# Kernel optimization log

Hardware: AMD Instinct MI355X
Metric: run time of the kernel (lower is better)

## Reference

```python
import jax, jax.numpy as jnp
import numpy as np

N_NODES = 30000
IN_DIM = 8
HIDDEN = 64
HEADS1 = 8
OUT_DIM = 8
NEG_SLOPE = 0.2


def _glorot(key, shape):
    fan_in, fan_out = shape[0], shape[-1]
    lim = jnp.sqrt(6.0 / (fan_in + fan_out))
    return jax.random.uniform(key, shape, jnp.float32, -lim, lim)


def setup_inputs() -> dict:
    key = jax.random.key(0)
    ks = jax.random.split(key, 12)
    x = jax.random.normal(ks[0], (N_NODES, IN_DIM), jnp.float32)
    edge_index = jax.random.randint(ks[1], (2, 300000), 0, N_NODES, jnp.int32)
    # layer 1: in=8, out=HIDDEN per head, 8 heads, concat
    W1l = _glorot(ks[2], (IN_DIM, HEADS1 * HIDDEN))
    W1r = _glorot(ks[3], (IN_DIM, HEADS1 * HIDDEN))
    a1 = _glorot(ks[4], (HEADS1, HIDDEN))
    b1 = jnp.zeros((HEADS1 * HIDDEN,), jnp.float32)
    # layer 2: in=HEADS1*HIDDEN, out=OUT_DIM, 1 head
    W2l = _glorot(ks[5], (HEADS1 * HIDDEN, OUT_DIM))
    W2r = _glorot(ks[6], (HEADS1 * HIDDEN, OUT_DIM))
    a2 = _glorot(ks[7], (1, OUT_DIM))
    b2 = jnp.zeros((OUT_DIM,), jnp.float32)
    return {"x": x, "edge_index": edge_index, "W1l": W1l, "W1r": W1r,
            "a1": a1, "b1": b1, "W2l": W2l, "W2r": W2r, "a2": a2, "b2": b2}


def gatv2_layer(x, src, dst, Wl, Wr, att, bias, heads, out_ch):
    n = x.shape[0]
    xl = (x @ Wl).reshape(n, heads, out_ch)   # messages (source side)
    xr = (x @ Wr).reshape(n, heads, out_ch)   # target side
    h = jax.nn.leaky_relu(xl[src] + xr[dst], NEG_SLOPE)   # [E,H,C]
    e = jnp.einsum('ehc,hc->eh', h, att)                  # [E,H]
    # segment softmax over incoming edges per destination node
    m = jax.ops.segment_max(e, dst, num_segments=n)
    p = jnp.exp(e - m[dst])
    denom = jax.ops.segment_sum(p, dst, num_segments=n)
    alpha = p / denom[dst]                                # [E,H]
    out = jax.ops.segment_sum(alpha[..., None] * xl[src], dst, num_segments=n)
    return out.reshape(n, heads * out_ch) + bias


def reference(x, edge_index, W1l, W1r, a1, b1, W2l, W2r, a2, b2):
    n = x.shape[0]
    loops = jnp.arange(n, dtype=edge_index.dtype)
    src = jnp.concatenate([edge_index[0], loops])  # add_self_loops=True (PyG default)
    dst = jnp.concatenate([edge_index[1], loops])
    h = gatv2_layer(x, src, dst, W1l, W1r, a1, b1, HEADS1, HIDDEN)
    h = jax.nn.relu(h)
    out = gatv2_layer(h, src, dst, W2l, W2r, a2, b2, 1, OUT_DIM)
    return out
```

## Files before the change

kernel.cpp:

```cpp
#include <hip/hip_runtime.h>
#include <math.h>

#define N_NODES   30000
#define N_EDGE    300000
#define N_EDGE_T  330000
#define HEADS     8
#define HIDDEN    64
#define IN_DIM    8
#define OUT_DIM   8
#define NEG_SLOPE 0.2f

typedef float v2f __attribute__((ext_vector_type(2)));


__global__ __launch_bounds__(256) void count_kernel(const int* __restrict__ ei,
                                                    int* __restrict__ count) {
    int e = blockIdx.x * 256 + threadIdx.x;
    if (e >= N_EDGE_T) return;
    int d = (e < N_EDGE) ? ei[N_EDGE + e] : (e - N_EDGE);
    atomicAdd(&count[d], 1);
}

__global__ __launch_bounds__(1024) void scan_kernel(const int* __restrict__ count,
                                                    int* __restrict__ row_start,
                                                    int* __restrict__ cursor) {
    __shared__ int wsum[16];
    const int tid  = threadIdx.x;
    const int wave = tid >> 6;
    const int lane = tid & 63;
    const int4* c4 = (const int4*)count;
    const int N4 = N_NODES / 4;
    int run = 0;
    for (int r = 0; r < 4; ++r) {
        const int g  = r * 1024 + tid;
        const int i0 = 2 * g;
        const int i1 = 2 * g + 1;
        int4 v0 = make_int4(0,0,0,0), v1 = make_int4(0,0,0,0);
        if (i0 < N4) v0 = c4[i0];
        if (i1 < N4) v1 = c4[i1];
        int s = v0.x + v0.y + v0.z + v0.w + v1.x + v1.y + v1.z + v1.w;
        int sc = s;
        #pragma unroll
        for (int off = 1; off < 64; off <<= 1) {
            int t = __shfl_up(sc, off, 64);
            if (lane >= off) sc += t;
        }
        if (lane == 63) wsum[wave] = sc;
        __syncthreads();
        if (tid < 16) {
            int w = wsum[tid];
            #pragma unroll
            for (int off = 1; off < 16; off <<= 1) {
                int t = __shfl_up(w, off, 64);
                if (tid >= off) w += t;
            }
            wsum[tid] = w;
        }
        __syncthreads();
        const int woff = (wave > 0) ? wsum[wave - 1] : 0;
        int e0 = run + woff + (sc - s);
        int4 ex0, ex1;
        ex0.x = e0;           ex0.y = ex0.x + v0.x;
        ex0.z = ex0.y + v0.y; ex0.w = ex0.z + v0.z;
        int e4 = ex0.w + v0.w;
        ex1.x = e4;           ex1.y = ex1.x + v1.x;
        ex1.z = ex1.y + v1.y; ex1.w = ex1.z + v1.z;
        if (i0 < N4) { ((int4*)row_start)[i0] = ex0; ((int4*)cursor)[i0] = ex0; }
        if (i1 < N4) { ((int4*)row_start)[i1] = ex1; ((int4*)cursor)[i1] = ex1; }
        const int tot = wsum[15];
        __syncthreads();
        run += tot;
    }
    if (tid == 0) row_start[N_NODES] = run;
}

__global__ __launch_bounds__(256) void scatter_kernel(const int* __restrict__ ei,
                                                      int* __restrict__ cursor,
                                                      int* __restrict__ edge_src,
                                                      const float* __restrict__ x,
                                                      float* __restrict__ xg) {
    int e = blockIdx.x * 256 + threadIdx.x;
    if (e >= N_EDGE_T) return;
    int s, d;
    if (e < N_EDGE) { s = ei[e]; d = ei[N_EDGE + e]; }
    else            { s = d = e - N_EDGE; }
    int pos = atomicAdd(&cursor[d], 1);
    edge_src[pos] = s;
    const float4* xs = (const float4*)(x + s * IN_DIM);
    float4 a = xs[0], b = xs[1];
    float4* dst = (float4*)(xg + pos * IN_DIM);
    dst[0] = a; dst[1] = b;
}


__global__ __launch_bounds__(256, 4) void layer1_kernel(
    const float* __restrict__ x,
    const float* __restrict__ W1l, const float* __restrict__ W1r,
    const float* __restrict__ a1,  const float* __restrict__ b1,
    const float* __restrict__ W2l, const float* __restrict__ W2r,
    const int* __restrict__ row_start, const float* __restrict__ xg,
    float* __restrict__ xl2, float* __restrict__ xr2)
{
    const int lane  = threadIdx.x & 63;
    const int gwave = (blockIdx.x * 256 + threadIdx.x) >> 6;
    const int nwave = (gridDim.x * 256) >> 6;
    const int half  = gwave & 1;
    const int grp   = lane >> 4;
    const int c4    = lane & 15;
    const int head  = half * 4 + grp;
    const int colb  = head * HIDDEN + c4 * 4;

    v2f wl[IN_DIM][2];
    #pragma unroll
    for (int k = 0; k < IN_DIM; ++k) {
        const float4 l4 = *(const float4*)&W1l[k * 512 + colb];
        wl[k][0] = v2f{l4.x, l4.y};
        wl[k][1] = v2f{l4.z, l4.w};
    }
    v2f av0, av1;
    { const float4 a4 = *(const float4*)&a1[colb];
      av0 = v2f{a4.x, a4.y}; av1 = v2f{a4.z, a4.w}; }
    const float4 b4 = *(const float4*)&b1[colb];

    const float4* g = (const float4*)xg;

    for (int d = gwave >> 1; d < N_NODES; d += nwave >> 1) {
        const int rs = __builtin_amdgcn_readfirstlane(row_start[d]);
        const int re = __builtin_amdgcn_readfirstlane(row_start[d + 1]);

        v2f xr0 = v2f{0.f, 0.f}, xr1 = v2f{0.f, 0.f};
        #pragma unroll
        for (int k = 0; k < IN_DIM; ++k) {
            const float xv = x[d * IN_DIM + k];
            const float4 r4 = *(const float4*)&W1r[k * 512 + colb];
            v2f xs = {xv, xv};
            xr0 = __builtin_elementwise_fma(xs, v2f{r4.x, r4.y}, xr0);
            xr1 = __builtin_elementwise_fma(xs, v2f{r4.z, r4.w}, xr1);
        }

        float denom = 0.f;
        v2f acc0 = v2f{0.f, 0.f}, acc1 = v2f{0.f, 0.f};

        for (int base = rs; base < re; base += 4) {
            float xf[4][IN_DIM];
            #pragma unroll
            for (int e = 0; e < 4; ++e) {
                const float4 u0 = g[(base + e) * 2];
                const float4 u1 = g[(base + e) * 2 + 1];
                xf[e][0] = u0.x; xf[e][1] = u0.y; xf[e][2] = u0.z; xf[e][3] = u0.w;
                xf[e][4] = u1.x; xf[e][5] = u1.y; xf[e][6] = u1.z; xf[e][7] = u1.w;
            }

            v2f xl[4][2];
            #pragma unroll
            for (int e = 0; e < 4; ++e) { xl[e][0] = v2f{0.f, 0.f}; xl[e][1] = v2f{0.f, 0.f}; }
            #pragma unroll
            for (int k = 0; k < IN_DIM; ++k) {
                #pragma unroll
                for (int e = 0; e < 4; ++e) {
                    v2f xs = {xf[e][k], xf[e][k]};
                    xl[e][0] = __builtin_elementwise_fma(xs, wl[k][0], xl[e][0]);
                    xl[e][1] = __builtin_elementwise_fma(xs, wl[k][1], xl[e][1]);
                }
            }

            float eh[4];
            #pragma unroll
            for (int e = 0; e < 4; ++e) {
                v2f v0 = xl[e][0] + xr0;
                v2f v1 = xl[e][1] + xr1;
                v2f t0 = __builtin_elementwise_max(v0, v0 * NEG_SLOPE);
                v2f t1 = __builtin_elementwise_max(v1, v1 * NEG_SLOPE);
                v2f s2 = __builtin_elementwise_fma(av1, t1, av0 * t0);
                eh[e] = s2.x + s2.y;
            }
            #pragma unroll
            for (int off = 1; off < 16; off <<= 1) {
                #pragma unroll
                for (int e = 0; e < 4; ++e) eh[e] += __shfl_xor(eh[e], off, 64);
            }

            float p[4];
            #pragma unroll
            for (int e = 0; e < 4; ++e)
                p[e] = (base + e < re) ? __expf(eh[e]) : 0.f;

            denom += (p[0] + p[1]) + (p[2] + p[3]);
            #pragma unroll
            for (int e = 0; e < 4; ++e) {
                v2f ps = {p[e], p[e]};
                acc0 = __builtin_elementwise_fma(ps, xl[e][0], acc0);
                acc1 = __builtin_elementwise_fma(ps, xl[e][1], acc1);
            }
        }

        const float inv = 1.f / denom;
        float hv[4];
        hv[0] = fmaxf(acc0.x * inv + b4.x, 0.f);
        hv[1] = fmaxf(acc0.y * inv + b4.y, 0.f);
        hv[2] = fmaxf(acc1.x * inv + b4.z, 0.f);
        hv[3] = fmaxf(acc1.y * inv + b4.w, 0.f);

        float w[16];
        #pragma unroll
        for (int j = 0; j < 16; ++j) w[j] = 0.f;
        #pragma unroll
        for (int i = 0; i < 4; ++i) {
            const float4 l0 = *(const float4*)&W2l[(colb + i) * OUT_DIM];
            const float4 l1 = *(const float4*)&W2l[(colb + i) * OUT_DIM + 4];
            const float4 r0 = *(const float4*)&W2r[(colb + i) * OUT_DIM];
            const float4 r1 = *(const float4*)&W2r[(colb + i) * OUT_DIM + 4];
            w[0]  = fmaf(hv[i], l0.x, w[0]);  w[1]  = fmaf(hv[i], l0.y, w[1]);
            w[2]  = fmaf(hv[i], l0.z, w[2]);  w[3]  = fmaf(hv[i], l0.w, w[3]);
            w[4]  = fmaf(hv[i], l1.x, w[4]);  w[5]  = fmaf(hv[i], l1.y, w[5]);
            w[6]  = fmaf(hv[i], l1.z, w[6]);  w[7]  = fmaf(hv[i], l1.w, w[7]);
            w[8]  = fmaf(hv[i], r0.x, w[8]);  w[9]  = fmaf(hv[i], r0.y, w[9]);
            w[10] = fmaf(hv[i], r0.z, w[10]); w[11] = fmaf(hv[i], r0.w, w[11]);
            w[12] = fmaf(hv[i], r1.x, w[12]); w[13] = fmaf(hv[i], r1.y, w[13]);
            w[14] = fmaf(hv[i], r1.z, w[14]); w[15] = fmaf(hv[i], r1.w, w[15]);
        }
        {   const bool up = (c4 & 8) != 0;
            #pragma unroll
            for (int i = 0; i < 8; ++i) {
                float send = up ? w[i] : w[i + 8];
                float recv = __shfl_xor(send, 8, 64);
                w[i] = (up ? w[i + 8] : w[i]) + recv;
            } }
        {   const bool up = (c4 & 4) != 0;
            #pragma unroll
            for (int i = 0; i < 4; ++i) {
                float send = up ? w[i] : w[i + 4];
                float recv = __shfl_xor(send, 4, 64);
                w[i] = (up ? w[i + 4] : w[i]) + recv;
            } }
        {   const bool up = (c4 & 2) != 0;
            #pragma unroll
            for (int i = 0; i < 2; ++i) {
                float send = up ? w[i] : w[i + 2];
                float recv = __shfl_xor(send, 2, 64);
                w[i] = (up ? w[i + 2] : w[i]) + recv;
            } }
        {   const bool up = (c4 & 1) != 0;
            float send = up ? w[0] : w[1];
            float recv = __shfl_xor(send, 1, 64);
            w[0] = (up ? w[1] : w[0]) + recv;
        }
        w[0] += __shfl_xor(w[0], 16, 64);
        w[0] += __shfl_xor(w[0], 32, 64);
        if (lane < 16) {
            float* dst = (lane < 8) ? &xl2[d * OUT_DIM + lane]
                                    : &xr2[d * OUT_DIM + (lane - 8)];
            atomicAdd(dst, w[0]);
        }
    }
}


__global__ __launch_bounds__(256) void layer2_kernel(
    const float* __restrict__ xl2, const float* __restrict__ xr2,
    const float* __restrict__ a2,  const float* __restrict__ b2,
    const int* __restrict__ row_start, const int* __restrict__ edge_src,
    float* __restrict__ out)
{
    const int lane  = threadIdx.x & 63;
    const int gwave = (blockIdx.x * 256 + threadIdx.x) >> 6;
    const int nwave = (gridDim.x * 256) >> 6;
    const int sub = lane >> 3;
    const int c   = lane & 7;

    const float a_c = a2[c];
    const float b_c = b2[c];

    for (int d = gwave; d < N_NODES; d += nwave) {
        const float xr_d = xr2[d * OUT_DIM + c];
        const int rs = row_start[d];
        const int re = row_start[d + 1];

        float denom = 0.f, acc = 0.f;
        for (int base = rs; base < re; base += 8) {
            int e = base + sub;
            bool valid = (e < re);
            int s = valid ? edge_src[e] : 0;
            float xls = xl2[s * OUT_DIM + c];
            float v = xls + xr_d;
            float t = fmaxf(v, NEG_SLOPE * v);
            float eh = a_c * t;
            eh += __shfl_xor(eh, 1, 64);
            eh += __shfl_xor(eh, 2, 64);
            eh += __shfl_xor(eh, 4, 64);
            float p = valid ? __expf(eh) : 0.f;
            denom += p;
            acc = fmaf(p, xls, acc);
        }
        denom += __shfl_xor(denom, 8,  64);  acc += __shfl_xor(acc, 8,  64);
        denom += __shfl_xor(denom, 16, 64);  acc += __shfl_xor(acc, 16, 64);
        denom += __shfl_xor(denom, 32, 64);  acc += __shfl_xor(acc, 32, 64);
        if (sub == 0) out[d * OUT_DIM + c] = acc / denom + b_c;
    }
}


extern "C" void kernel_launch(void* const* d_in, const int* in_sizes, int n_in,
                              void* d_out, int out_size, void* d_ws, size_t ws_size,
                              hipStream_t stream) {
    const float* x   = (const float*)d_in[0];
    const int*   ei  = (const int*)  d_in[1];
    const float* W1l = (const float*)d_in[2];
    const float* W1r = (const float*)d_in[3];
    const float* a1  = (const float*)d_in[4];
    const float* b1  = (const float*)d_in[5];
    const float* W2l = (const float*)d_in[6];
    const float* W2r = (const float*)d_in[7];
    const float* a2  = (const float*)d_in[8];
    const float* b2  = (const float*)d_in[9];
    float* out = (float*)d_out;

    char* ws = (char*)d_ws;
    size_t off = 0;
    auto carve = [&](size_t bytes) { char* p = ws + off; off += (bytes + 255) & ~size_t(255); return p; };
    int*   count     = (int*)  carve(N_NODES * sizeof(int));
    float* xl2       = (float*)carve(N_NODES * OUT_DIM * sizeof(float));
    float* xr2       = (float*)carve(N_NODES * OUT_DIM * sizeof(float));
    size_t zero_span = off;
    int*   row_start = (int*)  carve((N_NODES + 1) * sizeof(int));
    int*   cursor    = (int*)  carve(N_NODES * sizeof(int));
    int*   edge_src  = (int*)  carve((N_EDGE_T + 8) * sizeof(int));
    float* xg        = (float*)carve((N_EDGE_T + 8) * IN_DIM * sizeof(float));

    hipMemsetAsync(count, 0, zero_span, stream);
    count_kernel  <<<(N_EDGE_T + 255) / 256, 256, 0, stream>>>(ei, count);
    scan_kernel   <<<1, 1024, 0, stream>>>(count, row_start, cursor);
    scatter_kernel<<<(N_EDGE_T + 255) / 256, 256, 0, stream>>>(ei, cursor, edge_src, x, xg);
    layer1_kernel <<<1024, 256, 0, stream>>>(x, W1l, W1r, a1, b1, W2l, W2r,
                                             row_start, xg, xl2, xr2);
    layer2_kernel <<<512, 256, 0, stream>>>(xl2, xr2, a2, b2,
                                            row_start, edge_src, out);
}
```

Before: 295.8 us.

## Process all heads per wave in layer1 and drop atomics for layer2 projection

Layer 1 now assigns one wave per destination node, with 8 columns per lane covering all 8 heads, instead of two waves each covering half the heads. This removes the cross-wave atomicAdd into xl2/xr2, replacing it with plain stores, and drops the zeroing of those buffers from the memset. Both node kernels switch from strided to contiguous block chunks, and the layer1 grid and occupancy hint are halved. Each lane now does twice the FMA work and holds more registers, which lowers occupancy and per-node parallelism in exchange for fewer atomics and less redundant xg reading.

Result: slower. 320.0 us (+8.2%).

```diff
diff --git a/kernel.cpp b/kernel.cpp
--- a/kernel.cpp
+++ b/kernel.cpp
@@ -93,7 +93,7 @@
 }
 
 
-__global__ __launch_bounds__(256, 4) void layer1_kernel(
+__global__ __launch_bounds__(256, 2) void layer1_kernel(
     const float* __restrict__ x,
     const float* __restrict__ W1l, const float* __restrict__ W1r,
     const float* __restrict__ a1,  const float* __restrict__ b1,
@@ -101,45 +101,56 @@
     const int* __restrict__ row_start, const float* __restrict__ xg,
     float* __restrict__ xl2, float* __restrict__ xr2)
 {
-    const int lane  = threadIdx.x & 63;
-    const int gwave = (blockIdx.x * 256 + threadIdx.x) >> 6;
-    const int nwave = (gridDim.x * 256) >> 6;
-    const int half  = gwave & 1;
-    const int grp   = lane >> 4;
-    const int c4    = lane & 15;
-    const int head  = half * 4 + grp;
-    const int colb  = head * HIDDEN + c4 * 4;
-
-    v2f wl[IN_DIM][2];
+    const int lane = threadIdx.x & 63;
+    const int wv   = threadIdx.x >> 6;
+    const int head = lane >> 3;
+    const int c8   = lane & 7;
+    const int colb = head * HIDDEN + c8 * 8;
+
+    v2f wl[IN_DIM][4];
     #pragma unroll
     for (int k = 0; k < IN_DIM; ++k) {
-        const float4 l4 = *(const float4*)&W1l[k * 512 + colb];
-        wl[k][0] = v2f{l4.x, l4.y};
-        wl[k][1] = v2f{l4.z, l4.w};
+        const float4 l0 = *(const float4*)&W1l[k * 512 + colb];
+        const float4 l1 = *(const float4*)&W1l[k * 512 + colb + 4];
+        wl[k][0] = v2f{l0.x, l0.y}; wl[k][1] = v2f{l0.z, l0.w};
+        wl[k][2] = v2f{l1.x, l1.y}; wl[k][3] = v2f{l1.z, l1.w};
     }
-    v2f av0, av1;
-    { const float4 a4 = *(const float4*)&a1[colb];
-      av0 = v2f{a4.x, a4.y}; av1 = v2f{a4.z, a4.w}; }
-    const float4 b4 = *(const float4*)&b1[colb];
+    v2f av[4];
+    { const float4 a0 = *(const float4*)&a1[colb];
+      const float4 a4 = *(const float4*)&a1[colb + 4];
+      av[0] = v2f{a0.x, a0.y}; av[1] = v2f{a0.z, a0.w};
+      av[2] = v2f{a4.x, a4.y}; av[3] = v2f{a4.z, a4.w}; }
+    float bb[8];
+    { const float4 b0 = *(const float4*)&b1[colb];
+      const float4 b4 = *(const float4*)&b1[colb + 4];
+      bb[0]=b0.x; bb[1]=b0.y; bb[2]=b0.z; bb[3]=b0.w;
+      bb[4]=b4.x; bb[5]=b4.y; bb[6]=b4.z; bb[7]=b4.w; }
+
+    const int chunk = (N_NODES + gridDim.x - 1) / gridDim.x;
+    const int dlo = blockIdx.x * chunk;
+    int dhi = dlo + chunk; if (dhi > N_NODES) dhi = N_NODES;
 
     const float4* g = (const float4*)xg;
 
-    for (int d = gwave >> 1; d < N_NODES; d += nwave >> 1) {
+    for (int d = dlo + wv; d < dhi; d += 4) {
         const int rs = __builtin_amdgcn_readfirstlane(row_start[d]);
         const int re = __builtin_amdgcn_readfirstlane(row_start[d + 1]);
 
-        v2f xr0 = v2f{0.f, 0.f}, xr1 = v2f{0.f, 0.f};
+        v2f xr[4] = {v2f{0.f,0.f}, v2f{0.f,0.f}, v2f{0.f,0.f}, v2f{0.f,0.f}};
         #pragma unroll
         for (int k = 0; k < IN_DIM; ++k) {
             const float xv = x[d * IN_DIM + k];
-            const float4 r4 = *(const float4*)&W1r[k * 512 + colb];
+            const float4 r0 = *(const float4*)&W1r[k * 512 + colb];
+            const float4 r1 = *(const float4*)&W1r[k * 512 + colb + 4];
             v2f xs = {xv, xv};
-            xr0 = __builtin_elementwise_fma(xs, v2f{r4.x, r4.y}, xr0);
-            xr1 = __builtin_elementwise_fma(xs, v2f{r4.z, r4.w}, xr1);
+            xr[0] = __builtin_elementwise_fma(xs, v2f{r0.x, r0.y}, xr[0]);
+            xr[1] = __builtin_elementwise_fma(xs, v2f{r0.z, r0.w}, xr[1]);
+            xr[2] = __builtin_elementwise_fma(xs, v2f{r1.x, r1.y}, xr[2]);
+            xr[3] = __builtin_elementwise_fma(xs, v2f{r1.z, r1.w}, xr[3]);
         }
 
         float denom = 0.f;
-        v2f acc0 = v2f{0.f, 0.f}, acc1 = v2f{0.f, 0.f};
+        v2f acc[4] = {v2f{0.f,0.f}, v2f{0.f,0.f}, v2f{0.f,0.f}, v2f{0.f,0.f}};
 
         for (int base = rs; base < re; base += 4) {
             float xf[4][IN_DIM];
@@ -151,9 +162,12 @@
                 xf[e][4] = u1.x; xf[e][5] = u1.y; xf[e][6] = u1.z; xf[e][7] = u1.w;
             }
 
-            v2f xl[4][2];
-            #pragma unroll
-            for (int e = 0; e < 4; ++e) { xl[e][0] = v2f{0.f, 0.f}; xl[e][1] = v2f{0.f, 0.f}; }
+            v2f xl[4][4];
+            #pragma unroll
+            for (int e = 0; e < 4; ++e) {
+                xl[e][0] = v2f{0.f,0.f}; xl[e][1] = v2f{0.f,0.f};
+                xl[e][2] = v2f{0.f,0.f}; xl[e][3] = v2f{0.f,0.f};
+            }
             #pragma unroll
             for (int k = 0; k < IN_DIM; ++k) {
                 #pragma unroll
@@ -161,21 +175,25 @@
                     v2f xs = {xf[e][k], xf[e][k]};
                     xl[e][0] = __builtin_elementwise_fma(xs, wl[k][0], xl[e][0]);
                     xl[e][1] = __builtin_elementwise_fma(xs, wl[k][1], xl[e][1]);
+                    xl[e][2] = __builtin_elementwise_fma(xs, wl[k][2], xl[e][2]);
+                    xl[e][3] = __builtin_elementwise_fma(xs, wl[k][3], xl[e][3]);
                 }
             }
 
             float eh[4];
             #pragma unroll
             for (int e = 0; e < 4; ++e) {
-                v2f v0 = xl[e][0] + xr0;
-                v2f v1 = xl[e][1] + xr1;
-                v2f t0 = __builtin_elementwise_max(v0, v0 * NEG_SLOPE);
-                v2f t1 = __builtin_elementwise_max(v1, v1 * NEG_SLOPE);
-                v2f s2 = __builtin_elementwise_fma(av1, t1, av0 * t0);
-                eh[e] = s2.x + s2.y;
-            }
-            #pragma unroll
-            for (int off = 1; off < 16; off <<= 1) {
+                v2f s = {0.f, 0.f};
+                #pragma unroll
+                for (int j = 0; j < 4; ++j) {
+                    v2f v = xl[e][j] + xr[j];
+                    v2f t = __builtin_elementwise_max(v, v * NEG_SLOPE);
+                    s = __builtin_elementwise_fma(av[j], t, s);
+                }
+                eh[e] = s.x + s.y;
+            }
+            #pragma unroll
+            for (int off = 1; off < 8; off <<= 1) {
                 #pragma unroll
                 for (int e = 0; e < 4; ++e) eh[e] += __shfl_xor(eh[e], off, 64);
             }
@@ -189,23 +207,29 @@
             #pragma unroll
             for (int e = 0; e < 4; ++e) {
                 v2f ps = {p[e], p[e]};
-                acc0 = __builtin_elementwise_fma(ps, xl[e][0], acc0);
-                acc1 = __builtin_elementwise_fma(ps, xl[e][1], acc1);
+                acc[0] = __builtin_elementwise_fma(ps, xl[e][0], acc[0]);
+                acc[1] = __builtin_elementwise_fma(ps, xl[e][1], acc[1]);
+                acc[2] = __builtin_elementwise_fma(ps, xl[e][2], acc[2]);
+                acc[3] = __builtin_elementwise_fma(ps, xl[e][3], acc[3]);
             }
         }
 
         const float inv = 1.f / denom;
-        float hv[4];
-        hv[0] = fmaxf(acc0.x * inv + b4.x, 0.f);
-        hv[1] = fmaxf(acc0.y * inv + b4.y, 0.f);
-        hv[2] = fmaxf(acc1.x * inv + b4.z, 0.f);
-        hv[3] = fmaxf(acc1.y * inv + b4.w, 0.f);
+        float hv[8];
+        hv[0] = fmaxf(acc[0].x * inv + bb[0], 0.f);
+        hv[1] = fmaxf(acc[0].y * inv + bb[1], 0.f);
+        hv[2] = fmaxf(acc[1].x * inv + bb[2], 0.f);
+        hv[3] = fmaxf(acc[1].y * inv + bb[3], 0.f);
+        hv[4] = fmaxf(acc[2].x * inv + bb[4], 0.f);
+        hv[5] = fmaxf(acc[2].y * inv + bb[5], 0.f);
+        hv[6] = fmaxf(acc[3].x * inv + bb[6], 0.f);
+        hv[7] = fmaxf(acc[3].y * inv + bb[7], 0.f);
 
         float w[16];
         #pragma unroll
         for (int j = 0; j < 16; ++j) w[j] = 0.f;
         #pragma unroll
-        for (int i = 0; i < 4; ++i) {
+        for (int i = 0; i < 8; ++i) {
             const float4 l0 = *(const float4*)&W2l[(colb + i) * OUT_DIM];
             const float4 l1 = *(const float4*)&W2l[(colb + i) * OUT_DIM + 4];
             const float4 r0 = *(const float4*)&W2r[(colb + i) * OUT_DIM];
@@ -219,38 +243,28 @@
             w[12] = fmaf(hv[i], r1.x, w[12]); w[13] = fmaf(hv[i], r1.y, w[13]);
             w[14] = fmaf(hv[i], r1.z, w[14]); w[15] = fmaf(hv[i], r1.w, w[15]);
         }
-        {   const bool up = (c4 & 8) != 0;
-            #pragma unroll
-            for (int i = 0; i < 8; ++i) {
-                float send = up ? w[i] : w[i + 8];
-                float recv = __shfl_xor(send, 8, 64);
-                w[i] = (up ? w[i + 8] : w[i]) + recv;
-            } }
-        {   const bool up = (c4 & 4) != 0;
-            #pragma unroll
-            for (int i = 0; i < 4; ++i) {
-                float send = up ? w[i] : w[i + 4];
-                float recv = __shfl_xor(send, 4, 64);
-                w[i] = (up ? w[i + 4] : w[i]) + recv;
-            } }
-        {   const bool up = (c4 & 2) != 0;
-            #pragma unroll
-            for (int i = 0; i < 2; ++i) {
-                float send = up ? w[i] : w[i + 2];
-                float recv = __shfl_xor(send, 2, 64);
-                w[i] = (up ? w[i + 2] : w[i]) + recv;
-            } }
-        {   const bool up = (c4 & 1) != 0;
-            float send = up ? w[0] : w[1];
-            float recv = __shfl_xor(send, 1, 64);
-            w[0] = (up ? w[1] : w[0]) + recv;
-        }
+        #pragma unroll
+        for (int r = 4; r >= 1; r >>= 1) {
+            const bool up = (c8 & r) != 0;
+            #pragma unroll
+            for (int i = 0; i < r; ++i) {
+                float sl = up ? w[i] : w[i + r];
+                float rl = __shfl_xor(sl, r, 64);
+                w[i] = (up ? w[i + r] : w[i]) + rl;
+                float sh = up ? w[8 + i] : w[8 + i + r];
+                float rh = __shfl_xor(sh, r, 64);
+                w[8 + i] = (up ? w[8 + i + r] : w[8 + i]) + rh;
+            }
+        }
+        w[0] += __shfl_xor(w[0], 8, 64);
         w[0] += __shfl_xor(w[0], 16, 64);
         w[0] += __shfl_xor(w[0], 32, 64);
-        if (lane < 16) {
-            float* dst = (lane < 8) ? &xl2[d * OUT_DIM + lane]
-                                    : &xr2[d * OUT_DIM + (lane - 8)];
-            atomicAdd(dst, w[0]);
+        w[8] += __shfl_xor(w[8], 8, 64);
+        w[8] += __shfl_xor(w[8], 16, 64);
+        w[8] += __shfl_xor(w[8], 32, 64);
+        if (head == 0) {
+            xl2[d * OUT_DIM + c8] = w[0];
+            xr2[d * OUT_DIM + c8] = w[8];
         }
     }
 }
@@ -262,16 +276,19 @@
     const int* __restrict__ row_start, const int* __restrict__ edge_src,
     float* __restrict__ out)
 {
-    const int lane  = threadIdx.x & 63;
-    const int gwave = (blockIdx.x * 256 + threadIdx.x) >> 6;
-    const int nwave = (gridDim.x * 256) >> 6;
+    const int lane = threadIdx.x & 63;
+    const int wv   = threadIdx.x >> 6;
     const int sub = lane >> 3;
     const int c   = lane & 7;
 
     const float a_c = a2[c];
     const float b_c = b2[c];
 
-    for (int d = gwave; d < N_NODES; d += nwave) {
+    const int chunk = (N_NODES + gridDim.x - 1) / gridDim.x;
+    const int dlo = blockIdx.x * chunk;
+    int dhi = dlo + chunk; if (dhi > N_NODES) dhi = N_NODES;
+
+    for (int d = dlo + wv; d < dhi; d += 4) {
         const float xr_d = xr2[d * OUT_DIM + c];
         const int rs = row_start[d];
         const int re = row_start[d + 1];
@@ -319,20 +336,19 @@
     size_t off = 0;
     auto carve = [&](size_t bytes) { char* p = ws + off; off += (bytes + 255) & ~size_t(255); return p; };
     int*   count     = (int*)  carve(N_NODES * sizeof(int));
-    float* xl2       = (float*)carve(N_NODES * OUT_DIM * sizeof(float));
-    float* xr2       = (float*)carve(N_NODES * OUT_DIM * sizeof(float));
-    size_t zero_span = off;
     int*   row_start = (int*)  carve((N_NODES + 1) * sizeof(int));
     int*   cursor    = (int*)  carve(N_NODES * sizeof(int));
     int*   edge_src  = (int*)  carve((N_EDGE_T + 8) * sizeof(int));
     float* xg        = (float*)carve((N_EDGE_T + 8) * IN_DIM * sizeof(float));
-
-    hipMemsetAsync(count, 0, zero_span, stream);
+    float* xl2       = (float*)carve(N_NODES * OUT_DIM * sizeof(float));
+    float* xr2       = (float*)carve(N_NODES * OUT_DIM * sizeof(float));
+
+    hipMemsetAsync(count, 0, N_NODES * sizeof(int), stream);
     count_kernel  <<<(N_EDGE_T + 255) / 256, 256, 0, stream>>>(ei, count);
     scan_kernel   <<<1, 1024, 0, stream>>>(count, row_start, cursor);
     scatter_kernel<<<(N_EDGE_T + 255) / 256, 256, 0, stream>>>(ei, cursor, edge_src, x, xg);
-    layer1_kernel <<<1024, 256, 0, stream>>>(x, W1l, W1r, a1, b1, W2l, W2r,
-                                             row_start, xg, xl2, xr2);
+    layer1_kernel <<<512, 256, 0, stream>>>(x, W1l, W1r, a1, b1, W2l, W2r,
+                                            row_start, xg, xl2, xr2);
     layer2_kernel <<<512, 256, 0, stream>>>(xl2, xr2, a2, b2,
                                             row_start, edge_src, out);
 }
```
